# Kernel optimization log

Measured on AMD Instinct MI355X. Metric: run time of the kernel, lower is better.

Reference implementation:

```python
import jax, jax.numpy as jnp
import numpy as np

SEQ_LEN = 2048   # configs.seq_len == h == KFSSM H
PRED_LEN = 720   # configs.pred_len == p
D_MODEL = 128    # configs.d_model == KFSSM N (complex state size N//2)
C_OUT = 64       # configs.c_out == channel dim of u
BATCH = 128


def setup_inputs() -> dict:
    key = jax.random.key(0)
    ks = jax.random.split(key, 12)
    H, n2, p = SEQ_LEN, D_MODEL // 2, PRED_LEN
    u = jax.random.normal(ks[0], (BATCH, SEQ_LEN, C_OUT), jnp.float32)
    x_mark_enc = jax.random.normal(ks[1], (BATCH, SEQ_LEN, 4), jnp.float32)
    x_dec = jax.random.normal(ks[2], (BATCH, PRED_LEN, C_OUT), jnp.float32)
    x_mark_dec = jax.random.normal(ks[3], (BATCH, PRED_LEN, 4), jnp.float32)
    # standard-normal noise; scaled by learned std inside reference (matches torch.normal(0, std))
    W_noise = jax.random.normal(ks[4], (BATCH, SEQ_LEN, C_OUT), jnp.float32)
    # Model params
    D = jax.random.normal(ks[5], (H,), jnp.float32)
    log_variance = jnp.log(1.0 + jax.random.uniform(ks[6], (1,), jnp.float32))
    # KFSSM params
    C_param = jax.random.normal(ks[7], (H, n2, 2), jnp.float32)  # view_as_real of complex C
    log_dt = (jax.random.uniform(ks[8], (H,), jnp.float32)
              * (np.log(0.1) - np.log(0.001)) + np.log(0.001))
    log_A_real = jnp.log(0.5 * jnp.ones((H, n2), jnp.float32))
    A_imag = np.pi * jnp.tile(jnp.arange(n2, dtype=jnp.float32)[None, :], (H, 1))
    # outporj: Linear(h -> 2p) then GLU(dim=2)
    proj_w = jax.random.normal(ks[9], (2 * p, H), jnp.float32) * 0.02
    proj_b = jnp.zeros((2 * p,), jnp.float32)
    return dict(u=u, x_mark_enc=x_mark_enc, x_dec=x_dec, x_mark_dec=x_mark_dec,
                W_noise=W_noise, D=D, log_variance=log_variance, C_param=C_param,
                log_dt=log_dt, log_A_real=log_A_real, A_imag=A_imag,
                proj_w=proj_w, proj_b=proj_b)


def _ssm_kernels(Nl, C_param, log_dt, log_A_real, A_imag):
    # KFSSM.forward(N=Nl): returns K, K2 of shape (H, Nl)
    dt = jnp.exp(log_dt)                              # (H,)
    C = C_param[..., 0] + 1j * C_param[..., 1]        # (H, n2)
    A = -jnp.exp(log_A_real) + 1j * A_imag            # (H, n2)
    ar = jnp.arange(Nl, dtype=log_dt.dtype)
    Bk = A[:, :1] * ar[None, :] * dt[:, None]         # (H, Nl) complex
    dtA = A * dt[:, None]                             # (H, n2)
    Kexp = jnp.exp(dtA[:, :, None] * ar[None, None, :])  # (H, n2, Nl)
    Cc = C * (jnp.exp(dtA) - 1.0) / A                 # (H, n2)
    K = 2.0 * jnp.einsum('hn,hnl->hl', Cc, Kexp).real # (H, Nl)
    K2 = 2.0 * (K * Bk).real                          # (H, Nl)
    return K, K2


def reference(u, x_mark_enc, x_dec, x_mark_dec, W_noise, D, log_variance,
              C_param, log_dt, log_A_real, A_imag, proj_w, proj_b):
    # instance normalization over time
    x_mean = jnp.mean(u, axis=1, keepdims=True)                  # (B,1,N)
    u0 = u - x_mean
    x_var = jnp.var(u0, axis=1, ddof=1, keepdims=True) + 1e-5    # unbiased, as torch.var
    un = u0 / jnp.sqrt(x_var)
    # Kalman process noise
    std = jnp.sqrt(jnp.exp(log_variance))                        # (1,)
    W = std * W_noise                                            # (B,L,N)
    l, Nch = un.shape[1], un.shape[2]
    nfft = 2 * l
    K, K2 = _ssm_kernels(Nch, C_param, log_dt, log_A_real, A_imag)  # (H=l, Nch)
    k_f = jnp.fft.rfft(K.T, n=nfft, axis=-1)                     # (Nch, l+1)
    k2_f = jnp.fft.rfft(K2.T, n=nfft, axis=-1)
    u_f = jnp.fft.rfft(jnp.transpose(un, (0, 2, 1)), n=nfft, axis=-1)   # (B,Nch,l+1)
    w_f = jnp.fft.rfft(jnp.transpose(W, (0, 2, 1)), n=nfft, axis=-1)
    y = (jnp.fft.irfft(u_f * k2_f, n=nfft, axis=-1)
         + jnp.fft.irfft(w_f * k_f, n=nfft, axis=-1))            # (B,Nch,2l)
    y = jnp.transpose(y, (0, 2, 1))[:, -l:, :] + un * D[:, None] # (B,l,Nch)
    # outporj: Linear(h->2p) over time axis, then GLU(dim=2); Dropout1d is identity at eval
    z = jnp.einsum('bnh,ph->bnp', jnp.transpose(y, (0, 2, 1)), proj_w) + proj_b  # (B,Nch,2p)
    a, b = jnp.split(z, 2, axis=2)
    y = jnp.transpose(a * jax.nn.sigmoid(b), (0, 2, 1))          # (B,p,Nch)
    y = y * jnp.sqrt(x_var) + x_mean
    return y[:, -PRED_LEN:, :]
```

## Files before the change

### kernel.cpp

```cpp
#include <hip/hip_runtime.h>
#include <math.h>

typedef unsigned short u16;
typedef unsigned int u32;
typedef __attribute__((ext_vector_type(8))) short short8;
typedef __attribute__((ext_vector_type(4))) float f32x4;

#define B_   128
#define L_   2048
#define C_   64
#define P_   720
#define P2_  1440
#define NPAD 1536
#define NFFT 4096
#define NROW (B_*C_)
#define TCHUNK 16

__device__ __forceinline__ u16 f2bf(float f) {
  union { float f; unsigned u; } x; x.f = f;
  unsigned r = x.u + 0x7fffu + ((x.u >> 16) & 1u);
  return (u16)(r >> 16);
}
__device__ __forceinline__ float bf2f_lo(u32 v) {
  union { unsigned u; float f; } x; x.u = v << 16; return x.f;
}
__device__ __forceinline__ float bf2f_hi(u32 v) {
  union { unsigned u; float f; } x; x.u = v & 0xffff0000u; return x.f;
}

__device__ __forceinline__ float2 cmul(float2 a, float2 b) {
  return make_float2(a.x * b.x - a.y * b.y, a.x * b.y + a.y * b.x);
}
__device__ __forceinline__ float2 cadd(float2 a, float2 b) { return make_float2(a.x + b.x, a.y + b.y); }
__device__ __forceinline__ float2 csub(float2 a, float2 b) { return make_float2(a.x - b.x, a.y - b.y); }

#define CSWAP(i, j) { float2 tt = a[i]; a[i] = a[j]; a[j] = tt; }

template<bool INV, bool HZ>
__device__ __forceinline__ void dft16(float2 a[16]) {
  const float S  = INV ? 1.f : -1.f;
  const float c1 = 0.9238795325112867f, s1 = 0.3826834323650898f, q2 = 0.7071067811865476f;
  const float2 W1 = make_float2( c1, S * s1), W2 = make_float2( q2, S * q2), W3 = make_float2( s1, S * c1);
  const float2 W5 = make_float2(-s1, S * c1), W6 = make_float2(-q2, S * q2), W7 = make_float2(-c1, S * s1);
  if (HZ) {
    a[8]  = a[0];
    a[9]  = cmul(a[1], W1);
    a[10] = cmul(a[2], W2);
    a[11] = cmul(a[3], W3);
    a[12] = make_float2(-S * a[4].y, S * a[4].x);
    a[13] = cmul(a[5], W5);
    a[14] = cmul(a[6], W6);
    a[15] = cmul(a[7], W7);
  } else {
    float2 t;
    t = csub(a[0], a[8]);  a[0] = cadd(a[0], a[8]);  a[8]  = t;
    t = csub(a[1], a[9]);  a[1] = cadd(a[1], a[9]);  a[9]  = cmul(t, W1);
    t = csub(a[2], a[10]); a[2] = cadd(a[2], a[10]); a[10] = cmul(t, W2);
    t = csub(a[3], a[11]); a[3] = cadd(a[3], a[11]); a[11] = cmul(t, W3);
    t = csub(a[4], a[12]); a[4] = cadd(a[4], a[12]); a[12] = make_float2(-S * t.y, S * t.x);
    t = csub(a[5], a[13]); a[5] = cadd(a[5], a[13]); a[13] = cmul(t, W5);
    t = csub(a[6], a[14]); a[6] = cadd(a[6], a[14]); a[14] = cmul(t, W6);
    t = csub(a[7], a[15]); a[7] = cadd(a[7], a[15]); a[15] = cmul(t, W7);
  }
#pragma unroll
  for (int h = 0; h < 16; h += 8) {
    float2 t;
    t = csub(a[h+0], a[h+4]); a[h+0] = cadd(a[h+0], a[h+4]); a[h+4] = t;
    t = csub(a[h+1], a[h+5]); a[h+1] = cadd(a[h+1], a[h+5]); a[h+5] = cmul(t, W2);
    t = csub(a[h+2], a[h+6]); a[h+2] = cadd(a[h+2], a[h+6]); a[h+6] = make_float2(-S * t.y, S * t.x);
    t = csub(a[h+3], a[h+7]); a[h+3] = cadd(a[h+3], a[h+7]); a[h+7] = cmul(t, W6);
  }
#pragma unroll
  for (int q = 0; q < 16; q += 4) {
    float2 t;
    t = csub(a[q+0], a[q+2]); a[q+0] = cadd(a[q+0], a[q+2]); a[q+2] = t;
    t = csub(a[q+1], a[q+3]); a[q+1] = cadd(a[q+1], a[q+3]); a[q+3] = make_float2(-S * t.y, S * t.x);
  }
#pragma unroll
  for (int p = 0; p < 16; p += 2) {
    float2 t = csub(a[p], a[p+1]); a[p] = cadd(a[p], a[p+1]); a[p+1] = t;
  }
  CSWAP(1, 8); CSWAP(2, 4); CSWAP(3, 12); CSWAP(5, 10); CSWAP(7, 14); CSWAP(11, 13);
}

__device__ __forceinline__ void twchain(float2 a[16], float2 w1) {
  float2 w2 = cmul(w1, w1);
  float2 w3 = cmul(w2, w1);
  float2 w4 = cmul(w2, w2);
  float2 w5 = cmul(w3, w2);
  float2 w6 = cmul(w3, w3);
  float2 w7 = cmul(w4, w3);
  float2 w8 = cmul(w4, w4);
  float2 w9 = cmul(w5, w4);
  float2 w10 = cmul(w5, w5);
  float2 w11 = cmul(w6, w5);
  float2 w12 = cmul(w6, w6);
  float2 w13 = cmul(w7, w6);
  float2 w14 = cmul(w7, w7);
  float2 w15 = cmul(w8, w7);
  a[1]  = cmul(a[1],  w1);  a[2]  = cmul(a[2],  w2);  a[3]  = cmul(a[3],  w3);
  a[4]  = cmul(a[4],  w4);  a[5]  = cmul(a[5],  w5);  a[6]  = cmul(a[6],  w6);
  a[7]  = cmul(a[7],  w7);  a[8]  = cmul(a[8],  w8);  a[9]  = cmul(a[9],  w9);
  a[10] = cmul(a[10], w10); a[11] = cmul(a[11], w11); a[12] = cmul(a[12], w12);
  a[13] = cmul(a[13], w13); a[14] = cmul(a[14], w14); a[15] = cmul(a[15], w15);
}

__device__ __forceinline__ void lds_wA(float2* X, const float2 r[16], int tid) {
  int base = (tid & 15) * 16 + ((tid >> 4) ^ ((tid & 7) << 1));
#pragma unroll
  for (int i = 0; i < 16; ++i) X[base + i * 256] = r[i];
}
__device__ __forceinline__ void lds_wB(float2* X, const float2 r[16], int tid) {
#pragma unroll
  for (int i = 0; i < 16; ++i)
    X[((tid & 0xF0) + i) * 16 + ((tid & 15) ^ ((i & 7) << 1))] = r[i];
}
__device__ __forceinline__ void lds_rd(const float2* X, float2 r[16], int tid) {
  const float4* X4 = (const float4*)X;
#pragma unroll
  for (int p = 0; p < 8; ++p) {
    float4 v = X4[tid * 8 + (p ^ (tid & 7))];
    r[2 * p]     = make_float2(v.x, v.y);
    r[2 * p + 1] = make_float2(v.z, v.w);
  }
}

__device__ __forceinline__ void fft_fwd_hz(float2 r[16], float2* X, int tid, const float2* twg) {
  dft16<false, true>(r);
  twchain(r, twg[tid]);
  lds_wA(X, r, tid);
  __syncthreads();
  lds_rd(X, r, tid);
  dft16<false, false>(r);
  twchain(r, twg[(tid & 15) << 4]);
  __syncthreads();
  lds_wB(X, r, tid);
  __syncthreads();
  lds_rd(X, r, tid);
  dft16<false, false>(r);
}

__device__ __forceinline__ void fft_inv(float2 r[16], float2* X, int tid, const float2* twg) {
  dft16<true, false>(r);
  __syncthreads();
  lds_wB(X, r, tid);
  __syncthreads();
  lds_rd(X, r, tid);
  float2 wb = twg[(tid & 15) << 4];
  twchain(r, make_float2(wb.x, -wb.y));
  dft16<true, false>(r);
  __syncthreads();
  lds_wA(X, r, tid);
  __syncthreads();
  lds_rd(X, r, tid);
  float2 wa = twg[tid];
  twchain(r, make_float2(wa.x, -wa.y));
  dft16<true, false>(r);
}

__global__ void k_twfill(float2* __restrict__ tw) {
  int k = threadIdx.x;
  double ang = -2.0 * 3.14159265358979323846 * (double)k / 4096.0;
  tw[k] = make_float2((float)cos(ang), (float)sin(ang));
}

__global__ void k_wconv(const float* __restrict__ pw, u16* __restrict__ wb) {
  size_t idx = (size_t)blockIdx.x * 256 + threadIdx.x;
  int n = (int)(idx >> 11);
  int k = (int)(idx & 2047);
  int q = n >> 1;
  float v = 0.f;
  if (q < P_) {
    int p = (n & 1) ? (P_ + q) : q;
    v = pw[(size_t)p * L_ + k];
  }
  wb[idx] = f2bf(v);
}

__global__ __launch_bounds__(256) void k_stats1(const float* __restrict__ u, float* __restrict__ ps,
                                                float* __restrict__ pq) {
  int blk = blockIdx.x;
  int b = blk >> 4, q = blk & 15;
  int tid = threadIdx.x;
  int c4 = tid & 15, g = tid >> 4;
  const float4* u4 = (const float4*)(u + ((size_t)b * L_ + q * 128) * C_);
  float4 s = make_float4(0.f, 0.f, 0.f, 0.f), sq = s;
#pragma unroll
  for (int i = 0; i < 8; ++i) {
    float4 v = u4[(size_t)(g + 16 * i) * 16 + c4];
    s.x += v.x; s.y += v.y; s.z += v.z; s.w += v.w;
    sq.x += v.x * v.x; sq.y += v.y * v.y; sq.z += v.z * v.z; sq.w += v.w * v.w;
  }
  __shared__ float4 sb[16][16], qb[16][16];
  sb[g][c4] = s; qb[g][c4] = sq;
  __syncthreads();
  if (g == 0) {
    float4 S = sb[0][c4], Q = qb[0][c4];
#pragma unroll
    for (int k = 1; k < 16; ++k) {
      float4 a = sb[k][c4], d = qb[k][c4];
      S.x += a.x; S.y += a.y; S.z += a.z; S.w += a.w;
      Q.x += d.x; Q.y += d.y; Q.z += d.z; Q.w += d.w;
    }
    ((float4*)ps)[blk * 16 + c4] = S;
    ((float4*)pq)[blk * 16 + c4] = Q;
  }
}

__global__ __launch_bounds__(256) void k_stats2(const float* __restrict__ ps, const float* __restrict__ pq,
                                                float4* __restrict__ mv) {
  int gid = blockIdx.x * 256 + threadIdx.x;
  int b = gid >> 6, c = gid & 63;
  float S = 0.f, Q = 0.f;
#pragma unroll
  for (int q = 0; q < 16; ++q) {
    S += ps[(size_t)(b * 16 + q) * 64 + c];
    Q += pq[(size_t)(b * 16 + q) * 64 + c];
  }
  float mean = S * (1.0f / 2048.0f);
  float var = (Q - S * S * (1.0f / 2048.0f)) * (1.0f / 2047.0f) + 1e-5f;
  float sv = sqrtf(var);
  mv[gid] = make_float4(mean, sv, 1.0f / sv, 0.0f);
}

__global__ __launch_bounds__(256) void k_ssmk(const float* __restrict__ Cp, const float* __restrict__ ldt,
                                              const float* __restrict__ lAr, const float* __restrict__ Aim,
                                              float2* __restrict__ kz) {
  int gid = blockIdx.x * 256 + threadIdx.x;
  int h = gid & 2047;
  int j = gid >> 11;
  float dt = expf(ldt[h]);
  float accx = 0.f;
  float Ar0 = 0.f;
  for (int n = 0; n < 64; ++n) {
    float Ar = -expf(lAr[h * 64 + n]);
    float Ai = Aim[h * 64 + n];
    if (n == 0) Ar0 = Ar;
    float dAr = Ar * dt, dAi = Ai * dt;
    float er = expf(dAr);
    float s1, c1; sincosf(dAi, &s1, &c1);
    float emr = er * c1 - 1.0f, emi = er * s1;
    float inv = 1.0f / (Ar * Ar + Ai * Ai);
    float qr = (emr * Ar + emi * Ai) * inv;
    float qi = (emi * Ar - emr * Ai) * inv;
    float cr = Cp[(size_t)(h * 64 + n) * 2];
    float ci = Cp[(size_t)(h * 64 + n) * 2 + 1];
    float ccr = cr * qr - ci * qi;
    float cci = cr * qi + ci * qr;
    float ej = expf(dAr * (float)j);
    float sj, cj; sincosf(dAi * (float)j, &sj, &cj);
    accx += ccr * (ej * cj) - cci * (ej * sj);
  }
  float K = 2.0f * accx;
  float K2 = 2.0f * K * (Ar0 * (float)j * dt);
  kz[(size_t)j * L_ + h] = make_float2(K2, -K);
}

__global__ __launch_bounds__(256) void k_packT(const float* __restrict__ u, const float* __restrict__ Wn,
                                               const float* __restrict__ lv, const float4* __restrict__ mv,
                                               u32* __restrict__ zu) {
  int b = blockIdx.x >> 5;
  int t0 = (blockIdx.x & 31) << 6;
  int tid = threadIdx.x;
  float stdn = sqrtf(__expf(lv[0]));
  __shared__ float2 tile[64][65];
  int c = tid & 63, r = tid >> 6;
  float4 m = mv[b * C_ + c];
#pragma unroll
  for (int i = 0; i < 16; ++i) {
    int t = t0 + i * 4 + r;
    size_t idx = ((size_t)b * L_ + t) * C_ + c;
    float uu = (u[idx] - m.x) * m.z;
    float ww = Wn[idx] * stdn;
    tile[i * 4 + r][c] = make_float2(uu, ww);
  }
  __syncthreads();
  int t = tid & 63, cb = tid >> 6;
#pragma unroll
  for (int i = 0; i < 16; ++i) {
    int c2 = i * 4 + cb;
    float2 v = tile[t][c2];
    zu[((size_t)(b * C_ + c2)) * L_ + t0 + t] = ((u32)f2bf(v.y) << 16) | (u32)f2bf(v.x);
  }
}

__global__ __launch_bounds__(256) void k_fftk(const float2* __restrict__ kz, const float2* __restrict__ twg,
                                              float2* __restrict__ G) {
  __shared__ float2 X[NFFT];
  int j = blockIdx.x, tid = threadIdx.x;
  float2 r[16];
#pragma unroll
  for (int n2 = 0; n2 < 8; ++n2) r[n2] = kz[(size_t)j * L_ + n2 * 256 + tid];
  fft_fwd_hz(r, X, tid, twg);
  const float sc = 1.0f / 8192.0f;
#pragma unroll
  for (int k0 = 0; k0 < 16; ++k0)
    G[(size_t)j * NFFT + k0 * 256 + tid] = make_float2(r[k0].x * sc, r[k0].y * sc);
}

__global__ __launch_bounds__(256) void k_fftmain(const u32* __restrict__ zu, const float2* __restrict__ twg,
                                                 const float2* __restrict__ G, const float* __restrict__ Dv,
                                                 u16* __restrict__ yT) {
  __shared__ float2 X[NFFT];
  int pair = blockIdx.x;
  int b = pair >> 5, j1 = pair & 31, j2 = j1 + 32;
  int row1 = b * 64 + j1, row2 = b * 64 + j2;
  int tid = threadIdx.x;
  float2 r[16];
  u32 Y1p[16];
  float usav1[8], usav2[8];
#pragma unroll
  for (int n2 = 0; n2 < 8; ++n2) {
    u32 v = zu[(size_t)row1 * L_ + n2 * 256 + tid];
    r[n2] = make_float2(bf2f_lo(v), bf2f_hi(v));
    usav1[n2] = r[n2].x;
  }
  fft_fwd_hz(r, X, tid, twg);
  const float2* G1 = G + (size_t)j1 * NFFT;
#pragma unroll
  for (int k0 = 0; k0 < 16; ++k0) {
    float2 y = cmul(r[k0], G1[k0 * 256 + tid]);
    Y1p[k0] = ((u32)f2bf(y.y) << 16) | (u32)f2bf(y.x);
  }
  __syncthreads();
#pragma unroll
  for (int n2 = 0; n2 < 8; ++n2) {
    u32 v = zu[(size_t)row2 * L_ + n2 * 256 + tid];
    r[n2] = make_float2(bf2f_lo(v), bf2f_hi(v));
    usav2[n2] = r[n2].x;
  }
  fft_fwd_hz(r, X, tid, twg);
  const float2* G2 = G + (size_t)j2 * NFFT;
#pragma unroll
  for (int k0 = 0; k0 < 16; ++k0) r[k0] = cmul(r[k0], G2[k0 * 256 + tid]);
  __syncthreads();
  int rr = (tid & 15) * 16 + (tid >> 4);
  int wsw = ((rr & 15) << 4) | (rr >> 4);
  int rp = (tid == 0) ? 0 : 256 - rr;
  int rsw = ((rp & 15) << 4) | (rp >> 4);
#pragma unroll
  for (int k0 = 0; k0 < 16; ++k0) {
    X[k0 * 256 + wsw] = make_float2(bf2f_lo(Y1p[k0]) + r[k0].y, r[k0].x - bf2f_hi(Y1p[k0]));
  }
  __syncthreads();
#pragma unroll
  for (int k0 = 0; k0 < 16; ++k0) {
    int k0p = (tid == 0) ? ((16 - k0) & 15) : (15 - k0);
    float2 Tm = X[k0p * 256 + rsw];
    r[k0] = make_float2(bf2f_lo(Y1p[k0]) - r[k0].y + Tm.x,
                        bf2f_hi(Y1p[k0]) + r[k0].x + Tm.y);
  }
  fft_inv(r, X, tid, twg);
#pragma unroll
  for (int n2 = 8; n2 < 16; ++n2) {
    int t = (n2 - 8) * 256 + tid;
    float d = Dv[t];
    yT[(size_t)row1 * L_ + t] = f2bf(r[n2].x + usav1[n2 - 8] * d);
    yT[(size_t)row2 * L_ + t] = f2bf(r[n2].y + usav2[n2 - 8] * d);
  }
}

__device__ __forceinline__ int lds_ix(int row, int slot) {
  return row * 32 + ((slot ^ ((row >> 1) & 3)) << 3);
}

__global__ __launch_bounds__(256) void k_gemm(const u16* __restrict__ A, const u16* __restrict__ B,
                                              const float* __restrict__ pb, const float4* __restrict__ mv,
                                              float* __restrict__ out) {
  __shared__ u16 As[128 * 32];
  __shared__ u16 Bs[128 * 32];
  __shared__ float ob[32 * 132];
  const int K = L_;
  int tid = threadIdx.x;
  int bid = blockIdx.x;
  int swz = (bid & 7) * 96 + (bid >> 3);
  int bm = swz % 64, bn = swz / 64;
  int wave = tid >> 6, lane = tid & 63;
  int wm = (wave >> 1) << 6, wn = (wave & 1) << 6;
  int lr = lane & 15, lk = lane >> 4;
  int trow = tid >> 2, tslot = tid & 3;
  const u16* Ag = A + (size_t)(bm * 128 + trow) * K + tslot * 8;
  const u16* Bg = B + (size_t)(bn * 128 + trow) * K + tslot * 8;
  f32x4 acc[4][4] = {};
  uint4 pa0 = *(const uint4*)(Ag);
  uint4 pa1 = *(const uint4*)(Ag + (size_t)64 * K);
  uint4 pb0 = *(const uint4*)(Bg);
  uint4 pb1 = *(const uint4*)(Bg + (size_t)64 * K);
  for (int kt = 0; kt < K; kt += 32) {
    __syncthreads();
    *(uint4*)&As[lds_ix(trow, tslot)] = pa0;
    *(uint4*)&As[lds_ix(trow + 64, tslot)] = pa1;
    *(uint4*)&Bs[lds_ix(trow, tslot)] = pb0;
    *(uint4*)&Bs[lds_ix(trow + 64, tslot)] = pb1;
    __syncthreads();
    if (kt + 32 < K) {
      pa0 = *(const uint4*)(Ag + kt + 32);
      pa1 = *(const uint4*)(Ag + (size_t)64 * K + kt + 32);
      pb0 = *(const uint4*)(Bg + kt + 32);
      pb1 = *(const uint4*)(Bg + (size_t)64 * K + kt + 32);
    }
    short8 af[4], bf[4];
#pragma unroll
    for (int i2 = 0; i2 < 4; ++i2) af[i2] = *(const short8*)&As[lds_ix(wm + i2 * 16 + lr, lk)];
#pragma unroll
    for (int j2 = 0; j2 < 4; ++j2) bf[j2] = *(const short8*)&Bs[lds_ix(wn + j2 * 16 + lr, lk)];
#pragma unroll
    for (int i2 = 0; i2 < 4; ++i2)
#pragma unroll
      for (int j2 = 0; j2 < 4; ++j2)
        acc[i2][j2] = __builtin_amdgcn_mfma_f32_16x16x32_bf16(af[i2], bf[j2], acc[i2][j2], 0, 0, 0);
  }
  int col_lo = wn + lr;
  for (int chunk = 0; chunk < 2; ++chunk) {
    __syncthreads();
#pragma unroll
    for (int j2c = 0; j2c < 2; ++j2c) {
      int j2 = chunk * 2 + j2c;
      int col = col_lo + j2 * 16;
      int nglob = bn * 128 + col;
      int q = nglob >> 1;
      float bias = 0.f;
      if (q < P_) bias = pb[(nglob & 1) ? (P_ + q) : q];
      int qloc = col >> 1;
      int s = (qloc & 15) | ((qloc >> 5) << 4);
#pragma unroll
      for (int i2 = 0; i2 < 4; ++i2) {
        int row = wm + i2 * 16 + lk * 4;
        float res[4];
#pragma unroll
        for (int rgi = 0; rgi < 4; ++rgi) {
          float val = acc[i2][j2][rgi] + bias;
          float other = __shfl_xor(val, 1);
          float4 m = mv[bm * 128 + row + rgi];
          res[rgi] = val * (1.0f / (1.0f + __expf(-other))) * m.y + m.x;
        }
        if (!(lane & 1)) {
          *(float4*)&ob[s * 132 + row] = make_float4(res[0], res[1], res[2], res[3]);
        }
      }
    }
    __syncthreads();
    int c = tid & 63, sl4 = tid >> 6;
    for (int rd = 0; rd < 16; ++rd) {
      int slice = rd * 4 + sl4;
      int s = slice >> 1, bb = slice & 1;
      int qloc = (s & 15) + chunk * 16 + ((s >> 4) << 5);
      int qglob = bn * 64 + qloc;
      if (qglob < P_) {
        int bg = bm * 2 + bb;
        out[((size_t)bg * P_ + qglob) * 64 + c] = ob[s * 132 + bb * 64 + c];
      }
    }
  }
}

extern "C" void kernel_launch(void* const* d_in, const int* in_sizes, int n_in,
                              void* d_out, int out_size, void* d_ws, size_t ws_size,
                              hipStream_t stream) {
  const float* u   = (const float*)d_in[0];
  const float* Wn  = (const float*)d_in[4];
  const float* Dv  = (const float*)d_in[5];
  const float* lv  = (const float*)d_in[6];
  const float* Cp  = (const float*)d_in[7];
  const float* ldt = (const float*)d_in[8];
  const float* lAr = (const float*)d_in[9];
  const float* Aim = (const float*)d_in[10];
  const float* pw  = (const float*)d_in[11];
  const float* pb  = (const float*)d_in[12];
  float* out = (float*)d_out;
  char* ws = (char*)d_ws;

  float2* tw = (float2*)(ws + 0);
  float4* mv = (float4*)(ws + (64 << 10));
  float2* G  = (float2*)(ws + (1 << 20));
  float2* kz = (float2*)(ws + (3 << 20));
  u16*    Wb = (u16*)   (ws + (4 << 20));
  float*  ps = (float*) (ws + (10 << 20));
  float*  pq = (float*) (ws + (10 << 20) + (512 << 10));
  u16*    yT = (u16*)   (ws + (16 << 20));
  u32*    zu = (u32*)   (ws + ((size_t)48 << 20));

  k_twfill<<<1, 256, 0, stream>>>(tw);
  k_wconv<<<(NPAD * L_) / 256, 256, 0, stream>>>(pw, Wb);
  k_stats1<<<B_ * TCHUNK, 256, 0, stream>>>(u, ps, pq);
  k_stats2<<<(B_ * C_) / 256, 256, 0, stream>>>(ps, pq, mv);
  k_ssmk<<<(C_ * L_) / 256, 256, 0, stream>>>(Cp, ldt, lAr, Aim, kz);
  k_packT<<<B_ * (L_ / 64), 256, 0, stream>>>(u, Wn, lv, mv, zu);
  k_fftk<<<C_, 256, 0, stream>>>(kz, tw, G);
  k_fftmain<<<NROW / 2, 256, 0, stream>>>(zu, tw, G, Dv, yT);
  k_gemm<<<64 * (NPAD / 128), 256, 0, stream>>>(yT, Wb, pb, mv, out);
}
```

Before: 351.2 us.

## Process one row per FFT block instead of packing two rows into one inverse FFT

The convolution kernel now handles a single (batch, channel) row per block. It does a forward FFT of the packed u/w complex signal, a pointwise multiply with the precomputed kernel spectrum, and an inverse FFT whose real part is kept. The earlier Hermitian-symmetry trick that merged two rows' spectra into one inverse FFT is removed, and the kernel spectrum scale is doubled to compensate. This drops the extra shared-memory shuffles, bf16 packing and register pressure, but costs two FFTs per row instead of one and a half, and launches twice as many blocks.

```diff
diff --git a/kernel.cpp b/kernel.cpp
--- a/kernel.cpp
+++ b/kernel.cpp
@@ -292,7 +292,7 @@
 #pragma unroll
   for (int n2 = 0; n2 < 8; ++n2) r[n2] = kz[(size_t)j * L_ + n2 * 256 + tid];
   fft_fwd_hz(r, X, tid, twg);
-  const float sc = 1.0f / 8192.0f;
+  const float sc = 1.0f / 4096.0f;
 #pragma unroll
   for (int k0 = 0; k0 < 16; ++k0)
     G[(size_t)j * NFFT + k0 * 256 + tid] = make_float2(r[k0].x * sc, r[k0].y * sc);
@@ -302,61 +302,28 @@
                                                  const float2* __restrict__ G, const float* __restrict__ Dv,
                                                  u16* __restrict__ yT) {
   __shared__ float2 X[NFFT];
-  int pair = blockIdx.x;
-  int b = pair >> 5, j1 = pair & 31, j2 = j1 + 32;
-  int row1 = b * 64 + j1, row2 = b * 64 + j2;
+  int row = blockIdx.x;
+  int j = row & 63;
   int tid = threadIdx.x;
   float2 r[16];
-  u32 Y1p[16];
-  float usav1[8], usav2[8];
+  float usav[8];
 #pragma unroll
   for (int n2 = 0; n2 < 8; ++n2) {
-    u32 v = zu[(size_t)row1 * L_ + n2 * 256 + tid];
-    r[n2] = make_float2(bf2f_lo(v), bf2f_hi(v));
-    usav1[n2] = r[n2].x;
+    u32 v = zu[(size_t)row * L_ + n2 * 256 + tid];
+    float uu = bf2f_lo(v), ww = bf2f_hi(v);
+    r[n2] = make_float2(uu, ww);
+    usav[n2] = uu;
   }
   fft_fwd_hz(r, X, tid, twg);
-  const float2* G1 = G + (size_t)j1 * NFFT;
-#pragma unroll
-  for (int k0 = 0; k0 < 16; ++k0) {
-    float2 y = cmul(r[k0], G1[k0 * 256 + tid]);
-    Y1p[k0] = ((u32)f2bf(y.y) << 16) | (u32)f2bf(y.x);
-  }
-  __syncthreads();
-#pragma unroll
-  for (int n2 = 0; n2 < 8; ++n2) {
-    u32 v = zu[(size_t)row2 * L_ + n2 * 256 + tid];
-    r[n2] = make_float2(bf2f_lo(v), bf2f_hi(v));
-    usav2[n2] = r[n2].x;
-  }
-  fft_fwd_hz(r, X, tid, twg);
-  const float2* G2 = G + (size_t)j2 * NFFT;
-#pragma unroll
-  for (int k0 = 0; k0 < 16; ++k0) r[k0] = cmul(r[k0], G2[k0 * 256 + tid]);
-  __syncthreads();
-  int rr = (tid & 15) * 16 + (tid >> 4);
-  int wsw = ((rr & 15) << 4) | (rr >> 4);
-  int rp = (tid == 0) ? 0 : 256 - rr;
-  int rsw = ((rp & 15) << 4) | (rp >> 4);
-#pragma unroll
-  for (int k0 = 0; k0 < 16; ++k0) {
-    X[k0 * 256 + wsw] = make_float2(bf2f_lo(Y1p[k0]) + r[k0].y, r[k0].x - bf2f_hi(Y1p[k0]));
-  }
-  __syncthreads();
-#pragma unroll
-  for (int k0 = 0; k0 < 16; ++k0) {
-    int k0p = (tid == 0) ? ((16 - k0) & 15) : (15 - k0);
-    float2 Tm = X[k0p * 256 + rsw];
-    r[k0] = make_float2(bf2f_lo(Y1p[k0]) - r[k0].y + Tm.x,
-                        bf2f_hi(Y1p[k0]) + r[k0].x + Tm.y);
-  }
+  const float2* Gj = G + (size_t)j * NFFT;
+#pragma unroll
+  for (int k0 = 0; k0 < 16; ++k0) r[k0] = cmul(r[k0], Gj[k0 * 256 + tid]);
   fft_inv(r, X, tid, twg);
 #pragma unroll
   for (int n2 = 8; n2 < 16; ++n2) {
     int t = (n2 - 8) * 256 + tid;
-    float d = Dv[t];
-    yT[(size_t)row1 * L_ + t] = f2bf(r[n2].x + usav1[n2 - 8] * d);
-    yT[(size_t)row2 * L_ + t] = f2bf(r[n2].y + usav2[n2 - 8] * d);
+    float yv = r[n2].x + usav[n2 - 8] * Dv[t];
+    yT[(size_t)row * L_ + t] = f2bf(yv);
   }
 }
 
@@ -487,6 +454,6 @@
   k_ssmk<<<(C_ * L_) / 256, 256, 0, stream>>>(Cp, ldt, lAr, Aim, kz);
   k_packT<<<B_ * (L_ / 64), 256, 0, stream>>>(u, Wn, lv, mv, zu);
   k_fftk<<<C_, 256, 0, stream>>>(kz, tw, G);
-  k_fftmain<<<NROW / 2, 256, 0, stream>>>(zu, tw, G, Dv, yT);
+  k_fftmain<<<NROW, 256, 0, stream>>>(zu, tw, G, Dv, yT);
   k_gemm<<<64 * (NPAD / 128), 256, 0, stream>>>(yT, Wb, pb, mv, out);
 }
```

New measurement: 343.1 us. 2.3% less time.
